# Kernel tuning notes

Hardware: AMD Instinct MI355X
Metric: run time of the kernel (lower is better)

## Reference

```python
import jax, jax.numpy as jnp
import numpy as np

B, S, N = 1, 8, 512
DV, DM = 256, 64
INNER, H, WS = 256, 8, 3
DH = INNER // H


def setup_inputs() -> dict:
    key = jax.random.key(0)
    ks = jax.random.split(key, 7)
    w = lambda k, shape: jax.random.normal(k, shape, dtype=jnp.float32) * 0.02
    return {
        "values": jax.random.normal(ks[0], (B, S, N, DV), dtype=jnp.float32),
        "metadata": jax.random.normal(ks[1], (B, S, N, DM), dtype=jnp.float32),
        "w_meta_outer": w(ks[2], (DM, 2 * INNER)),   # meta_to_qk of outer block
        "w_qkv": w(ks[3], (DV, 3 * INNER)),           # values_to_qkv (no bias)
        "w_meta_inner": w(ks[4], (DM, 2 * INNER)),   # meta_to_qk of inner block
        "w_out": w(ks[5], (INNER, DV)),               # output_proj Linear weight
        "b_out": jnp.zeros((DV,), dtype=jnp.float32), # output_proj Linear bias
    }


def _forward(values, metadata, w_meta_outer, w_qkv, w_meta_inner, w_out, b_out):
    # ---- outer: source-level metadata attention to pick top-WS windows ----
    meta_mean = metadata.mean(axis=2)                      # [B,S,DM]
    qm, km = jnp.split(meta_mean @ w_meta_outer, 2, axis=-1)
    qm = jnp.clip(qm, -5, 5)
    km = jnp.clip(km, -5, 5)
    dots = jnp.einsum('bqd,bkd->bqk', qm, km) * (INNER ** -0.5)
    meta_attn = jax.nn.softmax(dots, axis=-1) + 2.0 * jnp.eye(S, dtype=dots.dtype)
    _, top_idx = jax.lax.top_k(meta_attn, WS)              # [B,S,WS], sorted desc

    # ---- gather adaptive windows over the source axis ----
    bidx = jnp.arange(B)[:, None, None]
    win_vals = values[bidx, top_idx]                       # [B,S,WS,N,DV]
    win_meta = metadata[bidx, top_idx]                     # [B,S,WS,N,DM]

    # Keys/values over all WS*N window tokens; queries only for slot-0 tokens
    # (the original computes all queries then slices x[:,:,0]; softmax is
    # per-query so restricting queries gives identical math).
    kv_vals = win_vals.reshape(B * S, WS * N, DV)
    kv_meta = win_meta.reshape(B * S, WS * N, DM)
    q_vals = win_vals[:, :, 0].reshape(B * S, N, DV)
    q_meta = win_meta[:, :, 0].reshape(B * S, N, DM)

    # ---- inner: fused QpKp^T + QmKm^T attention ----
    qp = q_vals @ w_qkv[:, :INNER]
    kp = kv_vals @ w_qkv[:, INNER:2 * INNER]
    v = kv_vals @ w_qkv[:, 2 * INNER:]
    qm2 = q_meta @ w_meta_inner[:, :INNER]
    km2 = kv_meta @ w_meta_inner[:, INNER:]

    def heads(x):  # [bs, n, inner] -> [bs, H, n, DH]
        return x.reshape(x.shape[0], x.shape[1], H, DH).transpose(0, 2, 1, 3)

    qp, kp, v, qm2, km2 = map(heads, (qp, kp, v, qm2, km2))
    scale = DH ** -0.5
    scores = jnp.einsum('bhqd,bhkd->bhqk', jnp.clip(qp, -5, 5), jnp.clip(kp, -5, 5)) * scale
    scores = scores + jnp.einsum('bhqd,bhkd->bhqk', jnp.clip(qm2, -5, 5), jnp.clip(km2, -5, 5)) * scale
    attn = jax.nn.softmax(scores, axis=-1)                 # [B*S,H,N,WS*N]
    out = jnp.einsum('bhqk,bhkd->bhqd', attn, v)           # [B*S,H,N,DH]
    out = out.transpose(0, 2, 1, 3).reshape(B * S, N, INNER)
    out = out @ w_out + b_out                              # dropout=0 (eval)
    return out.reshape(B, S, N, DV)


def reference(values, metadata, w_meta_outer, w_qkv, w_meta_inner, w_out, b_out):
    return _forward(values, metadata, w_meta_outer, w_qkv, w_meta_inner, w_out, b_out)
```

## Files before the change

### kernel.cpp

```cpp
#include <hip/hip_runtime.h>
#include <hip/hip_bf16.h>

#define S_ 8
#define N_ 512
#define DV_ 256
#define DM_ 64
#define INNER_ 256
#define H_ 8
#define WS_ 3
#define DH_ 32

typedef __attribute__((ext_vector_type(8))) __bf16 bf16x8;
typedef __attribute__((ext_vector_type(4))) float f32x4;

__device__ __forceinline__ float clip5(float x) {
    return fminf(5.0f, fmaxf(-5.0f, x));
}
__device__ __forceinline__ unsigned short f2bf(float x) {
    __hip_bfloat16 h = __float2bfloat16(x);
    return *reinterpret_cast<unsigned short*>(&h);
}

__global__ __launch_bounds__(256) void prep(
    const float* __restrict__ w_qkv, const float* __restrict__ w_meta_inner,
    const float* __restrict__ w_out, const float* __restrict__ metadata,
    unsigned short* __restrict__ WqkvT, unsigned short* __restrict__ WmetaT,
    unsigned short* __restrict__ WoutT, float* __restrict__ mm)
{
    __shared__ float Tf[64][65];
    int b = blockIdx.x, tid = threadIdx.x;
    if (b < 72) {
        const float* src; unsigned short* dst; int Nsrc, Ktot, k0, n0;
        if (b < 48)      { src = w_qkv;        dst = WqkvT; Nsrc = 768; Ktot = 256; k0 = (b & 3) * 64; n0 = (b >> 2) * 64; }
        else if (b < 56) { src = w_meta_inner; dst = WmetaT; Nsrc = 512; Ktot = 64;  k0 = 0;            n0 = (b - 48) * 64; }
        else             { int t = b - 56; src = w_out; dst = WoutT; Nsrc = 256; Ktot = 256; k0 = (t & 3) * 64; n0 = (t >> 2) * 64; }
#pragma unroll
        for (int p = 0; p < 16; p++) {
            int i = p * 256 + tid; int r = i >> 6, cc = i & 63;
            Tf[r][cc] = src[(size_t)(k0 + r) * Nsrc + n0 + cc];
        }
        __syncthreads();
#pragma unroll
        for (int p = 0; p < 16; p++) {
            int i = p * 256 + tid; int r = i >> 6, cc = i & 63;
            dst[(size_t)(n0 + r) * Ktot + k0 + cc] = f2bf(Tf[cc][r]);
        }
    } else {
        int s = b - 72;
        int d = tid & 63, g = tid >> 6;
        const float* base = metadata + ((size_t)(s * N_) + g * 128) * DM_ + d;
        float acc = 0.f;
        for (int i = 0; i < 128; i++) acc += base[(size_t)i * DM_];
        float* red = &Tf[0][0];
        red[tid] = acc;
        __syncthreads();
        if (tid < 64)
            mm[s * 64 + tid] = (red[tid] + red[tid + 64] + red[tid + 128] + red[tid + 192]) * (1.0f / N_);
    }
}

template<int ROLE>
__device__ __forceinline__ void gemm_body(
    unsigned short* smem,
    const float* __restrict__ A, const unsigned short* __restrict__ Bt,
    unsigned short* __restrict__ Qc, unsigned short* __restrict__ Kc,
    unsigned short* __restrict__ Vt,
    int m0, int n0g, int tid)
{
    constexpr int K = (ROLE == 1) ? 64 : 256;
    constexpr int KP = K + 8;
    unsigned short* As = smem;
    unsigned short* Bs = smem + 64 * KP;

    for (int i = tid; i < 64 * (K / 4); i += 256) {
        int r = i / (K / 4), g = i % (K / 4);
        float4 x = *(const float4*)(A + (size_t)(m0 + r) * K + 4 * g);
        *(ushort4*)&As[r * KP + 4 * g] =
            make_ushort4(f2bf(x.x), f2bf(x.y), f2bf(x.z), f2bf(x.w));
    }
    for (int i = tid; i < 64 * (K / 8); i += 256) {
        int r = i / (K / 8), g = i % (K / 8);
        *(bf16x8*)&Bs[r * KP + 8 * g] =
            *(const bf16x8*)(Bt + (size_t)(n0g + r) * K + 8 * g);
    }
    __syncthreads();

    const int w = tid >> 6, lane = tid & 63, c = lane & 15, qd = lane >> 4;
    const int mb = (w >> 1) * 32, nb = (w & 1) * 32;
    f32x4 acc[2][2];
    const f32x4 z = {0.f, 0.f, 0.f, 0.f};
#pragma unroll
    for (int mt = 0; mt < 2; mt++)
#pragma unroll
        for (int nt = 0; nt < 2; nt++) acc[mt][nt] = z;

#pragma unroll
    for (int kk = 0; kk < K / 32; kk++) {
        bf16x8 a[2], bb[2];
#pragma unroll
        for (int mt = 0; mt < 2; mt++)
            a[mt] = *(const bf16x8*)&As[(mb + mt * 16 + c) * KP + kk * 32 + qd * 8];
#pragma unroll
        for (int nt = 0; nt < 2; nt++)
            bb[nt] = *(const bf16x8*)&Bs[(nb + nt * 16 + c) * KP + kk * 32 + qd * 8];
#pragma unroll
        for (int mt = 0; mt < 2; mt++)
#pragma unroll
            for (int nt = 0; nt < 2; nt++)
                acc[mt][nt] = __builtin_amdgcn_mfma_f32_16x16x32_bf16(
                    a[mt], bb[nt], acc[mt][nt], 0, 0, 0);
    }

#pragma unroll
    for (int mt = 0; mt < 2; mt++)
#pragma unroll
        for (int nt = 0; nt < 2; nt++)
#pragma unroll
            for (int r = 0; r < 4; r++) {
                int tok = m0 + mb + mt * 16 + qd * 4 + r;
                int n = n0g + nb + nt * 16 + c;
                float v = acc[mt][nt][r];
                if (ROLE == 0) {
                    if (n < 512) {
                        unsigned short* dst = (n < 256) ? Qc : Kc;
                        int p = n & 255;
                        dst[(size_t)tok * 512 + (p >> 5) * 64 + (p & 31)] = f2bf(clip5(v));
                    } else {
                        int vc = n - 512, h = vc >> 5, dh = vc & 31;
                        int s = tok >> 9, ntok = tok & 511;
                        Vt[(size_t)((s * 8 + h) * 32 + dh) * 512 + ntok] = f2bf(v);
                    }
                } else {
                    unsigned short* dst = (n < 256) ? Qc : Kc;
                    int p = n & 255;
                    dst[(size_t)tok * 512 + (p >> 5) * 64 + 32 + (p & 31)] = f2bf(clip5(v));
                }
            }
}

__global__ __launch_bounds__(256) void fused1(
    const float* __restrict__ values, const float* __restrict__ metadata,
    const unsigned short* __restrict__ WqkvT,
    const unsigned short* __restrict__ WmetaT,
    const float* __restrict__ mm_g, const float* __restrict__ w_meta_outer,
    unsigned short* __restrict__ Qc, unsigned short* __restrict__ Kc,
    unsigned short* __restrict__ Vt, int* __restrict__ topidx)
{
    __shared__ __align__(16) unsigned short smem[2 * 64 * 264];
    const int b = blockIdx.x, tid = threadIdx.x;

    if (b == 0) {
        float* mml  = (float*)smem;
        float* qmS  = mml + 512;
        float* kmS  = qmS + 2048;
        float* dots = kmS + 2048;
        for (int i = tid; i < 512; i += 256) mml[i] = mm_g[i];
        __syncthreads();
        for (int i = tid; i < S_ * 512; i += 256) {
            int s = i >> 9, c = i & 511;
            float acc = 0.0f;
            for (int k = 0; k < DM_; k++) acc += mml[s * 64 + k] * w_meta_outer[k * 512 + c];
            acc = clip5(acc);
            if (c < 256) qmS[s * 256 + c] = acc; else kmS[s * 256 + c - 256] = acc;
        }
        __syncthreads();
        if (tid < 64) {
            int qi = tid >> 3, ki = tid & 7;
            float acc = 0.0f;
            for (int j = 0; j < INNER_; j++) acc += qmS[qi * 256 + j] * kmS[ki * 256 + j];
            dots[qi * 8 + ki] = acc * 0.0625f;
        }
        __syncthreads();
        if (tid < S_) {
            int r = tid;
            float mx = -1e30f;
            for (int k = 0; k < S_; k++) mx = fmaxf(mx, dots[r * 8 + k]);
            float e[S_], sum = 0.0f;
            for (int k = 0; k < S_; k++) { e[k] = __expf(dots[r * 8 + k] - mx); sum += e[k]; }
            float vals[S_];
            for (int k = 0; k < S_; k++) vals[k] = e[k] / sum + (k == r ? 2.0f : 0.0f);
            bool used[S_];
            for (int k = 0; k < S_; k++) used[k] = false;
            for (int w = 0; w < WS_; w++) {
                float best = -1e30f; int bi = 0;
                for (int k = 0; k < S_; k++) {
                    if (!used[k] && vals[k] > best) { best = vals[k]; bi = k; }
                }
                used[bi] = true;
                topidx[r * WS_ + w] = bi;
            }
        }
    } else if (b <= 768) {
        int g = b - 1;
        gemm_body<0>(smem, values, WqkvT, Qc, Kc, Vt, (g & 63) * 64, (g >> 6) * 64, tid);
    } else {
        int g = b - 769;
        gemm_body<1>(smem, metadata, WmetaT, Qc, Kc, Vt, (g & 63) * 64, (g >> 6) * 64, tid);
    }
}

__global__ __launch_bounds__(256) void attn_mfma(
    const int* __restrict__ topidx,
    const unsigned short* __restrict__ Qc,
    const unsigned short* __restrict__ Kc,
    const unsigned short* __restrict__ Vt,
    unsigned short* __restrict__ AO)
{
    const int s   = blockIdx.x;
    const int h   = blockIdx.y;
    const int qt  = blockIdx.z;
    const int tid = threadIdx.x;
    const int w    = tid >> 6;
    const int lane = tid & 63;
    const int c    = lane & 15;
    const int qd   = lane >> 4;
    const float scale = 0.17677669529663687f;

    __shared__ __align__(16) unsigned short Pq[4][64][40];
    __shared__ __align__(16) float Of[4][32][66];
    __shared__ float Ml[4][2][64];

    const int src0 = topidx[s * WS_ + 0];
    const int srcs[3] = { topidx[s * WS_ + 0], topidx[s * WS_ + 1], topidx[s * WS_ + 2] };

    bf16x8 qf[4][2];
    {
        const unsigned short* qbase =
            Qc + (size_t)(src0 * N_ + qt * 64) * 512 + h * 64 + qd * 8;
#pragma unroll
        for (int qg = 0; qg < 4; qg++)
#pragma unroll
            for (int kc = 0; kc < 2; kc++)
                qf[qg][kc] = *reinterpret_cast<const bf16x8*>(
                    qbase + (size_t)(qg * 16 + c) * 512 + kc * 32);
    }

    f32x4 oacc[2][4];
    const f32x4 zero4 = {0.f, 0.f, 0.f, 0.f};
#pragma unroll
    for (int mg = 0; mg < 2; mg++)
#pragma unroll
        for (int qg = 0; qg < 4; qg++) oacc[mg][qg] = zero4;
    float mrun[4], lrun[4];
#pragma unroll
    for (int qg = 0; qg < 4; qg++) { mrun[qg] = -3.0e38f; lrun[qg] = 0.f; }

    for (int step = 0; step < 12; step++) {
        const int chunk = step * 4 + w;
        const int src = srcs[chunk >> 4];
        const int klocal = (chunk & 15) * 32;

        bf16x8 kf[2][2];
        const unsigned short* kbase =
            Kc + (size_t)(src * N_ + klocal) * 512 + h * 64 + qd * 8;
#pragma unroll
        for (int mg = 0; mg < 2; mg++)
#pragma unroll
            for (int kc = 0; kc < 2; kc++)
                kf[mg][kc] = *reinterpret_cast<const bf16x8*>(
                    kbase + (size_t)(mg * 16 + c) * 512 + kc * 32);

        bf16x8 vf[2];
        const unsigned short* vbase =
            Vt + (size_t)((src * H_ + h) * DH_) * N_ + klocal + qd * 8;
#pragma unroll
        for (int mg = 0; mg < 2; mg++)
            vf[mg] = *reinterpret_cast<const bf16x8*>(vbase + (size_t)(mg * 16 + c) * N_);

        f32x4 sacc[2][4];
#pragma unroll
        for (int mg = 0; mg < 2; mg++)
#pragma unroll
            for (int qg = 0; qg < 4; qg++) sacc[mg][qg] = zero4;
#pragma unroll
        for (int kc = 0; kc < 2; kc++)
#pragma unroll
            for (int mg = 0; mg < 2; mg++)
#pragma unroll
                for (int qg = 0; qg < 4; qg++)
                    sacc[mg][qg] = __builtin_amdgcn_mfma_f32_16x16x32_bf16(
                        kf[mg][kc], qf[qg][kc], sacc[mg][qg], 0, 0, 0);

#pragma unroll
        for (int qg = 0; qg < 4; qg++) {
            float mx = sacc[0][qg][0];
#pragma unroll
            for (int r = 1; r < 4; r++) mx = fmaxf(mx, sacc[0][qg][r]);
#pragma unroll
            for (int r = 0; r < 4; r++) mx = fmaxf(mx, sacc[1][qg][r]);
            mx = fmaxf(mx, __shfl_xor(mx, 16));
            mx = fmaxf(mx, __shfl_xor(mx, 32));
            float mnew = fmaxf(mrun[qg], mx);
            float alpha = __expf((mrun[qg] - mnew) * scale);
            float msc = mnew * scale;
            float ps = 0.f;
            unsigned short pb[2][4];
#pragma unroll
            for (int mg = 0; mg < 2; mg++)
#pragma unroll
                for (int r = 0; r < 4; r++) {
                    float p = __expf(__builtin_fmaf(sacc[mg][qg][r], scale, -msc));
                    ps += p;
                    pb[mg][r] = f2bf(p);
                }
            ps += __shfl_xor(ps, 16);
            ps += __shfl_xor(ps, 32);
            lrun[qg] = lrun[qg] * alpha + ps;
            mrun[qg] = mnew;
#pragma unroll
            for (int mg = 0; mg < 2; mg++)
#pragma unroll
                for (int r = 0; r < 4; r++) oacc[mg][qg][r] *= alpha;
#pragma unroll
            for (int mg = 0; mg < 2; mg++) {
                ushort4 u = make_ushort4(pb[mg][0], pb[mg][1], pb[mg][2], pb[mg][3]);
                *reinterpret_cast<ushort4*>(&Pq[w][qg * 16 + c][mg * 16 + qd * 4]) = u;
            }
        }

        bf16x8 pf[4];
#pragma unroll
        for (int qg = 0; qg < 4; qg++)
            pf[qg] = *reinterpret_cast<const bf16x8*>(&Pq[w][qg * 16 + c][qd * 8]);
#pragma unroll
        for (int mg = 0; mg < 2; mg++)
#pragma unroll
            for (int qg = 0; qg < 4; qg++)
                oacc[mg][qg] = __builtin_amdgcn_mfma_f32_16x16x32_bf16(
                    vf[mg], pf[qg], oacc[mg][qg], 0, 0, 0);
    }

    __syncthreads();
#pragma unroll
    for (int qg = 0; qg < 4; qg++) {
        if (qd == 0) {
            Ml[w][0][qg * 16 + c] = mrun[qg];
            Ml[w][1][qg * 16 + c] = lrun[qg];
        }
#pragma unroll
        for (int mg = 0; mg < 2; mg++)
#pragma unroll
            for (int r = 0; r < 4; r++)
                Of[w][mg * 16 + qd * 4 + r][qg * 16 + c] = oacc[mg][qg][r];
    }
    __syncthreads();

    {
        int q = tid & 63;
        int dh0 = (tid >> 6) * 8;
        float mw[4], cw[4];
#pragma unroll
        for (int v = 0; v < 4; v++) mw[v] = Ml[v][0][q];
        float M = fmaxf(fmaxf(mw[0], mw[1]), fmaxf(mw[2], mw[3]));
        float L = 0.f;
#pragma unroll
        for (int v = 0; v < 4; v++) {
            cw[v] = __expf((mw[v] - M) * scale);
            L += cw[v] * Ml[v][1][q];
        }
        float inv = 1.0f / L;
        unsigned short* aorow =
            AO + (size_t)(s * N_ + qt * 64 + q) * 256 + h * 32 + dh0;
        unsigned short ub[8];
#pragma unroll
        for (int j = 0; j < 8; j++) {
            int dh = dh0 + j;
            float o = cw[0] * Of[0][dh][q] + cw[1] * Of[1][dh][q]
                    + cw[2] * Of[2][dh][q] + cw[3] * Of[3][dh][q];
            ub[j] = f2bf(o * inv);
        }
        uint4 u;
        u.x = (unsigned)ub[0] | ((unsigned)ub[1] << 16);
        u.y = (unsigned)ub[2] | ((unsigned)ub[3] << 16);
        u.z = (unsigned)ub[4] | ((unsigned)ub[5] << 16);
        u.w = (unsigned)ub[6] | ((unsigned)ub[7] << 16);
        *reinterpret_cast<uint4*>(aorow) = u;
    }
}

__global__ __launch_bounds__(256) void gemm_out(
    const unsigned short* __restrict__ AO, const unsigned short* __restrict__ Bt,
    const float* __restrict__ bias, float* __restrict__ outp)
{
    constexpr int K = 256;
    constexpr int KP = K + 8;
    __shared__ __align__(16) unsigned short As[64 * KP];
    __shared__ __align__(16) unsigned short Bs[64 * KP];
    const int tid = threadIdx.x;
    const int m0 = blockIdx.x * 64;
    const int n0g = blockIdx.y * 64;

    for (int i = tid; i < 64 * (K / 8); i += 256) {
        int r = i / (K / 8), g = i % (K / 8);
        *(bf16x8*)&As[r * KP + 8 * g] =
            *(const bf16x8*)(AO + (size_t)(m0 + r) * K + 8 * g);
    }
    for (int i = tid; i < 64 * (K / 8); i += 256) {
        int r = i / (K / 8), g = i % (K / 8);
        *(bf16x8*)&Bs[r * KP + 8 * g] =
            *(const bf16x8*)(Bt + (size_t)(n0g + r) * K + 8 * g);
    }
    __syncthreads();

    const int w = tid >> 6, lane = tid & 63, c = lane & 15, qd = lane >> 4;
    const int mb = (w >> 1) * 32, nb = (w & 1) * 32;
    f32x4 acc[2][2];
    const f32x4 z = {0.f, 0.f, 0.f, 0.f};
#pragma unroll
    for (int mt = 0; mt < 2; mt++)
#pragma unroll
        for (int nt = 0; nt < 2; nt++) acc[mt][nt] = z;

#pragma unroll
    for (int kk = 0; kk < K / 32; kk++) {
        bf16x8 a[2], bb[2];
#pragma unroll
        for (int mt = 0; mt < 2; mt++)
            a[mt] = *(const bf16x8*)&As[(mb + mt * 16 + c) * KP + kk * 32 + qd * 8];
#pragma unroll
        for (int nt = 0; nt < 2; nt++)
            bb[nt] = *(const bf16x8*)&Bs[(nb + nt * 16 + c) * KP + kk * 32 + qd * 8];
#pragma unroll
        for (int mt = 0; mt < 2; mt++)
#pragma unroll
            for (int nt = 0; nt < 2; nt++)
                acc[mt][nt] = __builtin_amdgcn_mfma_f32_16x16x32_bf16(
                    a[mt], bb[nt], acc[mt][nt], 0, 0, 0);
    }

#pragma unroll
    for (int mt = 0; mt < 2; mt++)
#pragma unroll
        for (int nt = 0; nt < 2; nt++)
#pragma unroll
            for (int r = 0; r < 4; r++) {
                int tok = m0 + mb + mt * 16 + qd * 4 + r;
                int n = n0g + nb + nt * 16 + c;
                outp[(size_t)tok * 256 + n] = acc[mt][nt][r] + bias[n];
            }
}

extern "C" void kernel_launch(void* const* d_in, const int* in_sizes, int n_in,
                              void* d_out, int out_size, void* d_ws, size_t ws_size,
                              hipStream_t stream) {
    const float* values       = (const float*)d_in[0];
    const float* metadata     = (const float*)d_in[1];
    const float* w_meta_outer = (const float*)d_in[2];
    const float* w_qkv        = (const float*)d_in[3];
    const float* w_meta_inner = (const float*)d_in[4];
    const float* w_out        = (const float*)d_in[5];
    const float* b_out        = (const float*)d_in[6];
    float* out = (float*)d_out;

    char* ws = (char*)d_ws;
    int* topidx = (int*)ws;
    float* mm = (float*)(ws + 256);
    unsigned short* WqkvT  = (unsigned short*)(ws + 4096);
    unsigned short* WmetaT = WqkvT + (size_t)768 * 256;
    unsigned short* WoutT  = WmetaT + (size_t)512 * 64;
    unsigned short* Qc     = WoutT + (size_t)256 * 256;
    unsigned short* Kc     = Qc + (size_t)4096 * 512;
    unsigned short* Vt     = Kc + (size_t)4096 * 512;
    unsigned short* AO     = Vt + (size_t)8 * 8 * 32 * 512;

    prep<<<dim3(80), dim3(256), 0, stream>>>(
        w_qkv, w_meta_inner, w_out, metadata, WqkvT, WmetaT, WoutT, mm);
    fused1<<<dim3(1281), dim3(256), 0, stream>>>(
        values, metadata, WqkvT, WmetaT, mm, w_meta_outer, Qc, Kc, Vt, topidx);
    attn_mfma<<<dim3(8, 8, 8), dim3(256), 0, stream>>>(topidx, Qc, Kc, Vt, AO);
    gemm_out<<<dim3(64, 4), dim3(256), 0, stream>>>(AO, WoutT, b_out, out);
}
```

Before: 127.5 us.

## Drop prep kernel; convert and transpose weights inside GEMM tiles, compute meta mean in block 0

Removes the separate prep launch that pre-transposed and bf16-converted the weights and computed the metadata mean. Each GEMM block now reads fp32 weights directly and transposes them into shared memory while converting. Block 0 of fused1 computes the per-source metadata mean itself before the outer attention. This saves one kernel launch and one round trip through workspace. In exchange, weight conversion is repeated in every block, the shared-memory stores are scattered and may bank-conflict, and the serial block 0 does more work.

```diff
diff --git a/kernel.cpp b/kernel.cpp
--- a/kernel.cpp
+++ b/kernel.cpp
@@ -21,48 +21,10 @@
     return *reinterpret_cast<unsigned short*>(&h);
 }
 
-__global__ __launch_bounds__(256) void prep(
-    const float* __restrict__ w_qkv, const float* __restrict__ w_meta_inner,
-    const float* __restrict__ w_out, const float* __restrict__ metadata,
-    unsigned short* __restrict__ WqkvT, unsigned short* __restrict__ WmetaT,
-    unsigned short* __restrict__ WoutT, float* __restrict__ mm)
-{
-    __shared__ float Tf[64][65];
-    int b = blockIdx.x, tid = threadIdx.x;
-    if (b < 72) {
-        const float* src; unsigned short* dst; int Nsrc, Ktot, k0, n0;
-        if (b < 48)      { src = w_qkv;        dst = WqkvT; Nsrc = 768; Ktot = 256; k0 = (b & 3) * 64; n0 = (b >> 2) * 64; }
-        else if (b < 56) { src = w_meta_inner; dst = WmetaT; Nsrc = 512; Ktot = 64;  k0 = 0;            n0 = (b - 48) * 64; }
-        else             { int t = b - 56; src = w_out; dst = WoutT; Nsrc = 256; Ktot = 256; k0 = (t & 3) * 64; n0 = (t >> 2) * 64; }
-#pragma unroll
-        for (int p = 0; p < 16; p++) {
-            int i = p * 256 + tid; int r = i >> 6, cc = i & 63;
-            Tf[r][cc] = src[(size_t)(k0 + r) * Nsrc + n0 + cc];
-        }
-        __syncthreads();
-#pragma unroll
-        for (int p = 0; p < 16; p++) {
-            int i = p * 256 + tid; int r = i >> 6, cc = i & 63;
-            dst[(size_t)(n0 + r) * Ktot + k0 + cc] = f2bf(Tf[cc][r]);
-        }
-    } else {
-        int s = b - 72;
-        int d = tid & 63, g = tid >> 6;
-        const float* base = metadata + ((size_t)(s * N_) + g * 128) * DM_ + d;
-        float acc = 0.f;
-        for (int i = 0; i < 128; i++) acc += base[(size_t)i * DM_];
-        float* red = &Tf[0][0];
-        red[tid] = acc;
-        __syncthreads();
-        if (tid < 64)
-            mm[s * 64 + tid] = (red[tid] + red[tid + 64] + red[tid + 128] + red[tid + 192]) * (1.0f / N_);
-    }
-}
-
 template<int ROLE>
 __device__ __forceinline__ void gemm_body(
     unsigned short* smem,
-    const float* __restrict__ A, const unsigned short* __restrict__ Bt,
+    const float* __restrict__ A, const float* __restrict__ W, int ldw,
     unsigned short* __restrict__ Qc, unsigned short* __restrict__ Kc,
     unsigned short* __restrict__ Vt,
     int m0, int n0g, int tid)
@@ -78,10 +40,13 @@
         *(ushort4*)&As[r * KP + 4 * g] =
             make_ushort4(f2bf(x.x), f2bf(x.y), f2bf(x.z), f2bf(x.w));
     }
-    for (int i = tid; i < 64 * (K / 8); i += 256) {
-        int r = i / (K / 8), g = i % (K / 8);
-        *(bf16x8*)&Bs[r * KP + 8 * g] =
-            *(const bf16x8*)(Bt + (size_t)(n0g + r) * K + 8 * g);
+    for (int i = tid; i < K * 16; i += 256) {
+        int k = i >> 4, n4 = (i & 15) * 4;
+        float4 x = *(const float4*)(W + (size_t)k * ldw + n0g + n4);
+        Bs[(n4 + 0) * KP + k] = f2bf(x.x);
+        Bs[(n4 + 1) * KP + k] = f2bf(x.y);
+        Bs[(n4 + 2) * KP + k] = f2bf(x.z);
+        Bs[(n4 + 3) * KP + k] = f2bf(x.w);
     }
     __syncthreads();
 
@@ -140,9 +105,8 @@
 
 __global__ __launch_bounds__(256) void fused1(
     const float* __restrict__ values, const float* __restrict__ metadata,
-    const unsigned short* __restrict__ WqkvT,
-    const unsigned short* __restrict__ WmetaT,
-    const float* __restrict__ mm_g, const float* __restrict__ w_meta_outer,
+    const float* __restrict__ w_meta_outer, const float* __restrict__ w_qkv,
+    const float* __restrict__ w_meta_inner,
     unsigned short* __restrict__ Qc, unsigned short* __restrict__ Kc,
     unsigned short* __restrict__ Vt, int* __restrict__ topidx)
 {
@@ -151,11 +115,28 @@
 
     if (b == 0) {
         float* mml  = (float*)smem;
-        float* qmS  = mml + 512;
+        float* scr  = mml + 512;
+        float* qmS  = scr + 1024;
         float* kmS  = qmS + 2048;
         float* dots = kmS + 2048;
-        for (int i = tid; i < 512; i += 256) mml[i] = mm_g[i];
-        __syncthreads();
+        const int tg = tid >> 4, d4 = (tid & 15) * 4;
+        for (int s = 0; s < 8; s++) {
+            float4 acc = make_float4(0.f, 0.f, 0.f, 0.f);
+            const float* base = metadata + (size_t)s * N_ * DM_ + d4;
+            for (int t = tg; t < N_; t += 16) {
+                float4 x = *(const float4*)(base + (size_t)t * DM_);
+                acc.x += x.x; acc.y += x.y; acc.z += x.z; acc.w += x.w;
+            }
+            *(float4*)&scr[tg * 64 + d4] = acc;
+            __syncthreads();
+            if (tid < 64) {
+                float a = 0.f;
+#pragma unroll
+                for (int g = 0; g < 16; g++) a += scr[g * 64 + tid];
+                mml[s * 64 + tid] = a * (1.0f / (float)N_);
+            }
+            __syncthreads();
+        }
         for (int i = tid; i < S_ * 512; i += 256) {
             int s = i >> 9, c = i & 511;
             float acc = 0.0f;
@@ -192,10 +173,12 @@
         }
     } else if (b <= 768) {
         int g = b - 1;
-        gemm_body<0>(smem, values, WqkvT, Qc, Kc, Vt, (g & 63) * 64, (g >> 6) * 64, tid);
+        gemm_body<0>(smem, values, w_qkv, 768, Qc, Kc, Vt,
+                     (g & 63) * 64, (g >> 6) * 64, tid);
     } else {
         int g = b - 769;
-        gemm_body<1>(smem, metadata, WmetaT, Qc, Kc, Vt, (g & 63) * 64, (g >> 6) * 64, tid);
+        gemm_body<1>(smem, metadata, w_meta_inner, 512, Qc, Kc, Vt,
+                     (g & 63) * 64, (g >> 6) * 64, tid);
     }
 }
 
@@ -379,7 +362,7 @@
 }
 
 __global__ __launch_bounds__(256) void gemm_out(
-    const unsigned short* __restrict__ AO, const unsigned short* __restrict__ Bt,
+    const unsigned short* __restrict__ AO, const float* __restrict__ w_out,
     const float* __restrict__ bias, float* __restrict__ outp)
 {
     constexpr int K = 256;
@@ -395,10 +378,13 @@
         *(bf16x8*)&As[r * KP + 8 * g] =
             *(const bf16x8*)(AO + (size_t)(m0 + r) * K + 8 * g);
     }
-    for (int i = tid; i < 64 * (K / 8); i += 256) {
-        int r = i / (K / 8), g = i % (K / 8);
-        *(bf16x8*)&Bs[r * KP + 8 * g] =
-            *(const bf16x8*)(Bt + (size_t)(n0g + r) * K + 8 * g);
+    for (int i = tid; i < K * 16; i += 256) {
+        int k = i >> 4, n4 = (i & 15) * 4;
+        float4 x = *(const float4*)(w_out + (size_t)k * 256 + n0g + n4);
+        Bs[(n4 + 0) * KP + k] = f2bf(x.x);
+        Bs[(n4 + 1) * KP + k] = f2bf(x.y);
+        Bs[(n4 + 2) * KP + k] = f2bf(x.z);
+        Bs[(n4 + 3) * KP + k] = f2bf(x.w);
     }
     __syncthreads();
 
@@ -454,19 +440,13 @@
 
     char* ws = (char*)d_ws;
     int* topidx = (int*)ws;
-    float* mm = (float*)(ws + 256);
-    unsigned short* WqkvT  = (unsigned short*)(ws + 4096);
-    unsigned short* WmetaT = WqkvT + (size_t)768 * 256;
-    unsigned short* WoutT  = WmetaT + (size_t)512 * 64;
-    unsigned short* Qc     = WoutT + (size_t)256 * 256;
-    unsigned short* Kc     = Qc + (size_t)4096 * 512;
-    unsigned short* Vt     = Kc + (size_t)4096 * 512;
-    unsigned short* AO     = Vt + (size_t)8 * 8 * 32 * 512;
-
-    prep<<<dim3(80), dim3(256), 0, stream>>>(
-        w_qkv, w_meta_inner, w_out, metadata, WqkvT, WmetaT, WoutT, mm);
+    unsigned short* Qc = (unsigned short*)(ws + 256);
+    unsigned short* Kc = Qc + (size_t)4096 * 512;
+    unsigned short* Vt = Kc + (size_t)4096 * 512;
+    unsigned short* AO = Vt + (size_t)8 * 8 * 32 * 512;
+
     fused1<<<dim3(1281), dim3(256), 0, stream>>>(
-        values, metadata, WqkvT, WmetaT, mm, w_meta_outer, Qc, Kc, Vt, topidx);
+        values, metadata, w_meta_outer, w_qkv, w_meta_inner, Qc, Kc, Vt, topidx);
     attn_mfma<<<dim3(8, 8, 8), dim3(256), 0, stream>>>(topidx, Qc, Kc, Vt, AO);
-    gemm_out<<<dim3(64, 4), dim3(256), 0, stream>>>(AO, WoutT, b_out, out);
-}
+    gemm_out<<<dim3(64, 4), dim3(256), 0, stream>>>(AO, w_out, b_out, out);
+}
```

Measured after the change: 186.6 us. 1.46x slower.
